# Kernel tuning notes

Measured on AMD Instinct MI355X. Metric: run time of the kernel, lower is better.

Reference implementation:

```python
import jax, jax.numpy as jnp
import numpy as np

NUM_STEPS = 32
SEQ = 64
IN = 512
HID = 256
NUM_CLASSES = 10
BATCH = 2048


def _lstm_layer(xseq, Wih, Whh, bih, bhh):
    # xseq: (T, B, D). PyTorch LSTMCell gate order: i, f, g, o.
    B = xseq.shape[1]
    H = Whh.shape[1]
    h0 = jnp.zeros((B, H), xseq.dtype)
    c0 = jnp.zeros((B, H), xseq.dtype)
    b = bih + bhh

    def step(carry, x):
        h, c = carry
        gates = x @ Wih.T + h @ Whh.T + b  # (B, 4H)
        i, f, g, o = jnp.split(gates, 4, axis=-1)
        c_new = jax.nn.sigmoid(f) * c + jax.nn.sigmoid(i) * jnp.tanh(g)
        h_new = jax.nn.sigmoid(o) * jnp.tanh(c_new)
        return (h_new, c_new), h_new

    (hT, cT), hs = jax.lax.scan(step, (h0, c0), xseq)
    return hs, hT


def _run_stack(xseq, layer_params):
    hT = None
    for (Wih, Whh, bih, bhh) in layer_params:
        xseq, hT = _lstm_layer(xseq, Wih, Whh, bih, bhh)
    return hT


def setup_inputs() -> dict:
    key = jax.random.key(0)
    ks = jax.random.split(key, 32)
    d = {"xs": jax.random.normal(ks[0], (BATCH, SEQ, IN), dtype=jnp.float32)}
    cfg = [IN, HID, HID]
    ki = 1
    for direc in ("f", "r"):
        for l, (di, dh) in enumerate(zip(cfg[:-1], cfg[1:])):
            s = 1.0 / np.sqrt(dh)
            d[f"Wih_{direc}{l}"] = jax.random.uniform(ks[ki], (4 * dh, di), minval=-s, maxval=s); ki += 1
            d[f"Whh_{direc}{l}"] = jax.random.uniform(ks[ki], (4 * dh, dh), minval=-s, maxval=s); ki += 1
            d[f"bih_{direc}{l}"] = jax.random.uniform(ks[ki], (4 * dh,), minval=-s, maxval=s); ki += 1
            d[f"bhh_{direc}{l}"] = jax.random.uniform(ks[ki], (4 * dh,), minval=-s, maxval=s); ki += 1
    s = 1.0 / np.sqrt(2 * HID)
    d["W3"] = jax.random.uniform(ks[ki], (NUM_CLASSES, 2 * HID), minval=-s, maxval=s); ki += 1
    d["b3"] = jax.random.uniform(ks[ki], (NUM_CLASSES,), minval=-s, maxval=s)
    return d


def reference(xs, Wih_f0, Whh_f0, bih_f0, bhh_f0, Wih_f1, Whh_f1, bih_f1, bhh_f1,
              Wih_r0, Whh_r0, bih_r0, bhh_r0, Wih_r1, Whh_r1, bih_r1, bhh_r1, W3, b3):
    # forward direction: timesteps 62-NUM_STEPS .. 61
    xf = jnp.transpose(xs[:, 62 - NUM_STEPS:62, :], (1, 0, 2))  # (T, B, D)
    hF = _run_stack(xf, [(Wih_f0, Whh_f0, bih_f0, bhh_f0),
                         (Wih_f1, Whh_f1, bih_f1, bhh_f1)])
    # reverse direction: last 3 frames in order 63, 62, 61
    xr = jnp.transpose(jnp.flip(xs[:, 61:64, :], axis=1), (1, 0, 2))  # (3, B, D)
    hR = _run_stack(xr, [(Wih_r0, Whh_r0, bih_r0, bhh_r0),
                         (Wih_r1, Whh_r1, bih_r1, bhh_r1)])
    latent = jnp.concatenate([hF, hR], axis=1)  # (B, 512)
    return latent @ W3.T + b3
```

## Files before the change

### kernel.cpp

```cpp
#include <hip/hip_runtime.h>
#include <stdint.h>

typedef unsigned short u16;
typedef unsigned long long u64;
typedef __attribute__((ext_vector_type(8)))  short  bf16x8;
typedef __attribute__((ext_vector_type(8)))  u16    u16x8;
typedef __attribute__((ext_vector_type(4)))  float  f32x4;
typedef __attribute__((ext_vector_type(16))) _Float16 f16x16;

#define MFMA_BF16(a,b,c) __builtin_amdgcn_mfma_f32_16x16x32_bf16((a),(b),(c),0,0,0)

#define BATCH   2048
#define FSTEPS  32
#define RSTEPS  3
#define NVF     35

static constexpr size_t HROW32 = 128;
static constexpr size_t HPAR32 = (size_t)BATCH * HROW32;

static constexpr size_t OFF_CTL  = 0;
static constexpr size_t OFF_H0G  = 32768;
static constexpr size_t OFF_H1G  = OFF_H0G + HPAR32 * 2 * 4;
static constexpr size_t OFF_LAT  = OFF_H1G + HPAR32 * 2 * 4;
static constexpr size_t OFF_XP   = OFF_LAT + (size_t)BATCH * 512 * 4;
static constexpr size_t XP_BYTES = (size_t)NVF * BATCH * 1024 * 2;
static constexpr size_t OFF_W0XF = OFF_XP + XP_BYTES;
static constexpr size_t OFF_W0XR = OFF_W0XF + (size_t)1024 * 512 * 2;
static constexpr size_t OFF_P0F  = OFF_W0XR + (size_t)1024 * 512 * 2;
static constexpr size_t OFF_P0R  = OFF_P0F + (size_t)32768 * 16;
static constexpr size_t OFF_P1F  = OFF_P0R + (size_t)32768 * 16;
static constexpr size_t OFF_P1R  = OFF_P1F + (size_t)65536 * 16;
static constexpr size_t OFF_BS0F = OFF_P1R + (size_t)65536 * 16;
static constexpr size_t OFF_BS0R = OFF_BS0F + 4096;
static constexpr size_t OFF_BS1F = OFF_BS0R + 4096;
static constexpr size_t OFF_BS1R = OFF_BS1F + 4096;
static constexpr size_t WS_NEED  = OFF_BS1R + 4096;

__device__ __forceinline__ u16 f2bf(float f) {
    unsigned u = __float_as_uint(f);
    unsigned r = (u + 0x7fffu + ((u >> 16) & 1u)) >> 16;
    return (u16)r;
}
__device__ __forceinline__ float sigm(float x) { return 1.0f / (1.0f + __expf(-x)); }
__device__ __forceinline__ float tanh_fast(float x) {
    float a = fabsf(x);
    float e = __expf(-2.0f * a);
    float t = (1.0f - e) / (1.0f + e);
    return x < 0.0f ? -t : t;
}

__device__ __forceinline__ bf16x8 ldsA(const char* H, int row, int k) {
    int byte = (row << 9) + (k << 1);
    byte ^= (row & 7) << 4;
    return *(const bf16x8*)(H + byte);
}

__device__ __forceinline__ void reload32(char* Hs, const u64* src, int rg, int tid) {
    u64 v[8];
#pragma unroll
    for (int i = 0; i < 8; ++i) {
        int idx = tid + (i << 8);
        v[i] = __hip_atomic_load(src + ((size_t)rg * 32 + (idx >> 6)) * 64 + (idx & 63),
                                 __ATOMIC_RELAXED, __HIP_MEMORY_SCOPE_AGENT);
    }
#pragma unroll
    for (int i = 0; i < 8; ++i) {
        int idx = tid + (i << 8);
        int row = idx >> 6, cu = idx & 63;
        int byte = (row << 9) + (cu << 3);
        byte ^= (row & 7) << 4;
        *(u64*)(Hs + byte) = v[i];
    }
}

__global__ void __launch_bounds__(256)
lstm_seq(const _Float16* __restrict__ xp,
         const u16* __restrict__ P0f_, const u16* __restrict__ P0r_,
         const u16* __restrict__ P1f_, const u16* __restrict__ P1r_,
         const float* __restrict__ bs1f, const float* __restrict__ bs1r,
         unsigned* __restrict__ h0g, unsigned* __restrict__ h1g,
         float* __restrict__ latent, unsigned* __restrict__ ctl)
{
    __shared__ char T0[16384];
    __shared__ char T1[16384];
    const int tid = threadIdx.x, wq = tid >> 6, lane = tid & 63;
    const int bid = blockIdx.x;
    const int colq = bid >> 6;
    const int rg   = bid & 63;
    const int mem  = colq * 4 + wq;
    const int hc   = mem * 16 + (lane & 15);
    const int klane = lane >> 4, q4 = klane << 2;
    unsigned* flag = ctl + (size_t)rg * 64;
    unsigned bcount = 0;

    for (int dir = 0; dir < 2; ++dir) {
        const int nst = dir ? RSTEPS : FSTEPS;
        const int gbase = dir ? FSTEPS : 0;
        const bf16x8* P0v = (const bf16x8*)(dir ? P0r_ : P0f_) + (size_t)mem * (8 * 4 * 64);
        const bf16x8* P1v = (const bf16x8*)(dir ? P1r_ : P1f_) + (size_t)mem * (16 * 4 * 64);
        const float* bs1 = dir ? bs1r : bs1f;
        float b1reg[4];
#pragma unroll
        for (int g = 0; g < 4; ++g) b1reg[g] = bs1[g * 256 + hc];

        float c0[2][4], c1[2][4];
#pragma unroll
        for (int Mt = 0; Mt < 2; ++Mt)
#pragma unroll
            for (int r = 0; r < 4; ++r) { c0[Mt][r] = 0.f; c1[Mt][r] = 0.f; }

        __syncthreads();
#pragma unroll
        for (int i = 0; i < 4; ++i) {
            ((f32x4*)T0)[i * 256 + tid] = (f32x4){0.f, 0.f, 0.f, 0.f};
            ((f32x4*)T1)[i * 256 + tid] = (f32x4){0.f, 0.f, 0.f, 0.f};
        }
        __syncthreads();

        f16x16 xqm[2];
#pragma unroll
        for (int Mt = 0; Mt < 2; ++Mt)
            xqm[Mt] = *(const f16x16*)(xp +
                ((((size_t)gbase * 128 + rg * 2 + Mt) * 16 + mem) * 64 + lane) * 16);

        for (int t = 0; t <= nst; ++t) {
            f32x4 acc1[4][2];
            if (t >= 1) {
#pragma unroll
                for (int g = 0; g < 4; ++g) { acc1[g][0] = (f32x4){0.f,0.f,0.f,0.f}; acc1[g][1] = (f32x4){0.f,0.f,0.f,0.f}; }
#pragma unroll
                for (int kc = 0; kc < 8; ++kc) {
                    bf16x8 a0 = ldsA(T0, (lane & 15),       kc * 32 + klane * 8);
                    bf16x8 a1 = ldsA(T0, 16 + (lane & 15),  kc * 32 + klane * 8);
#pragma unroll
                    for (int g = 0; g < 4; ++g) {
                        bf16x8 b = P1v[(kc * 4 + g) * 64 + lane];
                        acc1[g][0] = MFMA_BF16(a0, b, acc1[g][0]);
                        acc1[g][1] = MFMA_BF16(a1, b, acc1[g][1]);
                    }
                }
                if (t >= 2) {
#pragma unroll
                    for (int kc = 0; kc < 8; ++kc) {
                        bf16x8 a0 = ldsA(T1, (lane & 15),      kc * 32 + klane * 8);
                        bf16x8 a1 = ldsA(T1, 16 + (lane & 15), kc * 32 + klane * 8);
#pragma unroll
                        for (int g = 0; g < 4; ++g) {
                            bf16x8 b = P1v[((kc + 8) * 4 + g) * 64 + lane];
                            acc1[g][0] = MFMA_BF16(a0, b, acc1[g][0]);
                            acc1[g][1] = MFMA_BF16(a1, b, acc1[g][1]);
                        }
                    }
                }
            }

            f32x4 acc0[4][2];
            if (t < nst) {
#pragma unroll
                for (int g = 0; g < 4; ++g) { acc0[g][0] = (f32x4){0.f,0.f,0.f,0.f}; acc0[g][1] = (f32x4){0.f,0.f,0.f,0.f}; }
                if (t >= 1) {
#pragma unroll
                    for (int kc = 0; kc < 8; ++kc) {
                        bf16x8 a0 = ldsA(T0, (lane & 15),      kc * 32 + klane * 8);
                        bf16x8 a1 = ldsA(T0, 16 + (lane & 15), kc * 32 + klane * 8);
#pragma unroll
                        for (int g = 0; g < 4; ++g) {
                            bf16x8 b = P0v[(kc * 4 + g) * 64 + lane];
                            acc0[g][0] = MFMA_BF16(a0, b, acc0[g][0]);
                            acc0[g][1] = MFMA_BF16(a1, b, acc0[g][1]);
                        }
                    }
                }
            }

            if (t < nst) {
                unsigned* dst = h0g + (size_t)(t & 1) * HPAR32;
                const int cp = mem * 8 + ((lane & 15) >> 1);
#pragma unroll
                for (int Mt = 0; Mt < 2; ++Mt) {
                    float hn[4];
#pragma unroll
                    for (int r = 0; r < 4; ++r) {
                        float gi = acc0[0][Mt][r] + (float)xqm[Mt][0 * 4 + r];
                        float gf = acc0[1][Mt][r] + (float)xqm[Mt][1 * 4 + r];
                        float gg = acc0[2][Mt][r] + (float)xqm[Mt][2 * 4 + r];
                        float go = acc0[3][Mt][r] + (float)xqm[Mt][3 * 4 + r];
                        float cn = sigm(gf) * c0[Mt][r] + sigm(gi) * tanh_fast(gg);
                        c0[Mt][r] = cn;
                        hn[r] = sigm(go) * tanh_fast(cn);
                    }
                    const int rowbase = rg * 32 + Mt * 16 + q4;
#pragma unroll
                    for (int r = 0; r < 4; ++r) {
                        float p = __shfl_xor(hn[r], 1);
                        if (!(lane & 1)) {
                            unsigned w = (unsigned)f2bf(hn[r]) | ((unsigned)f2bf(p) << 16);
                            __hip_atomic_store(dst + (size_t)(rowbase + r) * HROW32 + cp, w,
                                               __ATOMIC_RELAXED, __HIP_MEMORY_SCOPE_AGENT);
                        }
                    }
                }
            }

            if (t >= 1) {
                const int cp = mem * 8 + ((lane & 15) >> 1);
#pragma unroll
                for (int Mt = 0; Mt < 2; ++Mt) {
                    float hn[4];
#pragma unroll
                    for (int r = 0; r < 4; ++r) {
                        float gi = acc1[0][Mt][r] + b1reg[0];
                        float gf = acc1[1][Mt][r] + b1reg[1];
                        float gg = acc1[2][Mt][r] + b1reg[2];
                        float go = acc1[3][Mt][r] + b1reg[3];
                        float cn = sigm(gf) * c1[Mt][r] + sigm(gi) * tanh_fast(gg);
                        c1[Mt][r] = cn;
                        hn[r] = sigm(go) * tanh_fast(cn);
                    }
                    const int rowbase = rg * 32 + Mt * 16 + q4;
                    if (t < nst) {
                        unsigned* dst = h1g + (size_t)((t - 1) & 1) * HPAR32;
#pragma unroll
                        for (int r = 0; r < 4; ++r) {
                            float p = __shfl_xor(hn[r], 1);
                            if (!(lane & 1)) {
                                unsigned w = (unsigned)f2bf(hn[r]) | ((unsigned)f2bf(p) << 16);
                                __hip_atomic_store(dst + (size_t)(rowbase + r) * HROW32 + cp, w,
                                                   __ATOMIC_RELAXED, __HIP_MEMORY_SCOPE_AGENT);
                            }
                        }
                    } else {
#pragma unroll
                        for (int r = 0; r < 4; ++r)
                            latent[(size_t)(rowbase + r) * 512 + dir * 256 + hc] = hn[r];
                    }
                }
            }

            if (t < nst) {
                ++bcount;
                asm volatile("s_waitcnt vmcnt(0)" ::: "memory");
                __syncthreads();
                if (tid == 0)
                    __hip_atomic_fetch_add(flag, 1u, __ATOMIC_RELAXED, __HIP_MEMORY_SCOPE_AGENT);
                if (t + 1 < nst) {
#pragma unroll
                    for (int Mt = 0; Mt < 2; ++Mt)
                        xqm[Mt] = *(const f16x16*)(xp +
                            ((((size_t)(gbase + t + 1) * 128 + rg * 2 + Mt) * 16 + mem) * 64 + lane) * 16);
                }
                if (tid == 0) {
                    while (__hip_atomic_load(flag, __ATOMIC_RELAXED, __HIP_MEMORY_SCOPE_AGENT)
                           < 4u * bcount) {}
                }
                __syncthreads();
                __builtin_amdgcn_sched_barrier(0);
                reload32(T0, (const u64*)(h0g + (size_t)(t & 1) * HPAR32), rg, tid);
                if (t >= 1)
                    reload32(T1, (const u64*)(h1g + (size_t)((t - 1) & 1) * HPAR32), rg, tid);
                __syncthreads();
            }
        }
    }
}

__global__ void __launch_bounds__(256)
xproj_gemm(const float* __restrict__ xs,
           const u16* __restrict__ W0xf, const u16* __restrict__ W0xr,
           const float* __restrict__ bs0f, const float* __restrict__ bs0r,
           _Float16* __restrict__ xp)
{
    __shared__ char As[16384];
    __shared__ char Bs[16384];
    const int tid = threadIdx.x, wv = tid >> 6, lane = tid & 63;
    const int phys = blockIdx.x;
    const int xcd = phys & 7, idx = phys >> 3;
    const int mt = xcd * 70 + (idx >> 3);
    const int nt = idx & 7;
    const int vf = mt >> 4;
    const int dirr = (vf >= 32);
    const int frame = dirr ? (95 - vf) : (30 + vf);
    const int brow = (mt & 15) * 128;
    const u16* Wp = (dirr ? W0xr : W0xf) + (size_t)nt * 128 * 512;
    const float* bs = dirr ? bs0r : bs0f;

    float breg[8];
#pragma unroll
    for (int n = 0; n < 8; ++n) breg[n] = bs[nt * 128 + n * 16 + (lane & 15)];

    f32x4 acc[8][2];
#pragma unroll
    for (int n = 0; n < 8; ++n) { acc[n][0] = (f32x4){0.f,0.f,0.f,0.f}; acc[n][1] = (f32x4){0.f,0.f,0.f,0.f}; }

    const int ar = tid >> 1, akoff = (tid & 1) * 32;
    const float* asrc0 = xs + ((size_t)(brow + ar) * 64 + frame) * 512 + akoff;

    for (int c = 0; c < 8; ++c) {
        {
            const float* s = asrc0 + c * 64;
            u16x8 o[4];
#pragma unroll
            for (int j2 = 0; j2 < 4; ++j2) {
                float4 f0 = *(const float4*)(s + j2 * 8);
                float4 f1 = *(const float4*)(s + j2 * 8 + 4);
                u16x8 o_;
                o_[0] = f2bf(f0.x); o_[1] = f2bf(f0.y); o_[2] = f2bf(f0.z); o_[3] = f2bf(f0.w);
                o_[4] = f2bf(f1.x); o_[5] = f2bf(f1.y); o_[6] = f2bf(f1.z); o_[7] = f2bf(f1.w);
                o[j2] = o_;
            }
#pragma unroll
            for (int j2 = 0; j2 < 4; ++j2) {
                int k = akoff + j2 * 8;
                int byte = (ar << 7) + (k << 1); byte ^= (ar & 7) << 4;
                *(u16x8*)(As + byte) = o[j2];
            }
        }
#pragma unroll
        for (int i = 0; i < 4; ++i) {
            int u = tid + i * 256;
            int ns = u >> 3, c8 = (u & 7) << 3;
            u16x8 v = *(const u16x8*)(Wp + (size_t)ns * 512 + c * 64 + c8);
            int byte = (ns << 7) + (c8 << 1); byte ^= (ns & 7) << 4;
            *(u16x8*)(Bs + byte) = v;
        }
        __syncthreads();
#pragma unroll
        for (int kk = 0; kk < 2; ++kk) {
            int kin = kk * 32 + (lane >> 4) * 8;
            bf16x8 a0, a1;
            int row = wv * 32 + (lane & 15);
            int byte = (row << 7) + (kin << 1); byte ^= (row & 7) << 4;
            a0 = *(const bf16x8*)(As + byte);
            int row1 = row + 16;
            byte = (row1 << 7) + (kin << 1); byte ^= (row1 & 7) << 4;
            a1 = *(const bf16x8*)(As + byte);
#pragma unroll
            for (int n = 0; n < 8; ++n) {
                int ns = n * 16 + (lane & 15);
                int bb = (ns << 7) + (kin << 1); bb ^= (ns & 7) << 4;
                bf16x8 bf_ = *(const bf16x8*)(Bs + bb);
                acc[n][0] = MFMA_BF16(a0, bf_, acc[n][0]);
                acc[n][1] = MFMA_BF16(a1, bf_, acc[n][1]);
            }
        }
        __syncthreads();
    }
#pragma unroll
    for (int n = 0; n < 8; ++n)
#pragma unroll
        for (int mm = 0; mm < 2; ++mm)
#pragma unroll
            for (int r = 0; r < 4; ++r) {
                int vm  = mt * 128 + wv * 32 + mm * 16 + ((lane >> 4) << 2) + r;
                int col = nt * 128 + n * 16 + (lane & 15);
                int vf2 = vm >> 11, brow2 = vm & 2047;
                int rb2 = brow2 >> 4, sub = brow2 & 15;
                int lane2 = ((sub >> 2) << 4) + (col & 15);
                int m2 = (col >> 4) & 15, g2 = col >> 8;
                size_t o = ((((size_t)vf2 * 128 + rb2) * 16 + m2) * 64 + lane2) * 16
                           + (g2 << 2) + (sub & 3);
                xp[o] = (_Float16)(acc[n][mm][r] + breg[n]);
            }
}

__global__ void pack_w(const float* __restrict__ Wa, int da,
                       const float* __restrict__ bi, const float* __restrict__ bh,
                       u16* __restrict__ Wout, float* __restrict__ bout)
{
    int total = 1024 * da;
    int gt = blockIdx.x * blockDim.x + threadIdx.x;
    int stride = gridDim.x * blockDim.x;
    for (int i = gt; i < total; i += stride) Wout[i] = f2bf(Wa[i]);
    if (bout && gt < 1024) bout[gt] = bi[gt] + bh[gt];
}

__global__ void pack_frag(const float* __restrict__ Wa, int da,
                          const float* __restrict__ Wb, int db,
                          int nkc, u16* __restrict__ out,
                          const float* __restrict__ bi, const float* __restrict__ bh,
                          float* __restrict__ bout)
{
    int total = 16 * nkc * 4 * 64;
    int gt = blockIdx.x * blockDim.x + threadIdx.x;
    int stride = gridDim.x * blockDim.x;
    for (int u = gt; u < total; u += stride) {
        int l = u & 63;
        int t1 = u >> 6;
        int g = t1 & 3;
        int t2 = t1 >> 2;
        int kc = t2 % nkc;
        int mem = t2 / nkc;
        int row = g * 256 + mem * 16 + (l & 15);
        int k0 = kc * 32 + ((l >> 4) << 3);
        u16x8 o;
#pragma unroll
        for (int jj = 0; jj < 8; ++jj) {
            int k = k0 + jj;
            float v = (k < da) ? Wa[(size_t)row * da + k] : Wb[(size_t)row * db + (k - da)];
            o[jj] = f2bf(v);
        }
        *(u16x8*)(out + (size_t)u * 8) = o;
    }
    if (bout && gt < 1024) bout[gt] = bi[gt] + bh[gt];
}

__global__ void final_linear(const float* __restrict__ latent, const float* __restrict__ W3,
                             const float* __restrict__ b3, float* __restrict__ out)
{
    int idx = blockIdx.x * blockDim.x + threadIdx.x;
    if (idx >= BATCH * 10) return;
    int bb = idx / 10, c = idx - bb * 10;
    const float* lrow = latent + (size_t)bb * 512;
    const float* wrow = W3 + (size_t)c * 512;
    float s = b3[c];
#pragma unroll 4
    for (int k = 0; k < 512; k += 4) {
        float4 lv = *(const float4*)(lrow + k);
        float4 wv = *(const float4*)(wrow + k);
        s += lv.x * wv.x + lv.y * wv.y + lv.z * wv.z + lv.w * wv.w;
    }
    out[idx] = s;
}

extern "C" void kernel_launch(void* const* d_in, const int* in_sizes, int n_in,
                              void* d_out, int out_size, void* d_ws, size_t ws_size,
                              hipStream_t stream)
{
    (void)in_sizes; (void)n_in; (void)out_size;
    if (ws_size < WS_NEED) return;

    const float* xs     = (const float*)d_in[0];
    const float* Wih_f0 = (const float*)d_in[1];
    const float* Whh_f0 = (const float*)d_in[2];
    const float* bih_f0 = (const float*)d_in[3];
    const float* bhh_f0 = (const float*)d_in[4];
    const float* Wih_f1 = (const float*)d_in[5];
    const float* Whh_f1 = (const float*)d_in[6];
    const float* bih_f1 = (const float*)d_in[7];
    const float* bhh_f1 = (const float*)d_in[8];
    const float* Wih_r0 = (const float*)d_in[9];
    const float* Whh_r0 = (const float*)d_in[10];
    const float* bih_r0 = (const float*)d_in[11];
    const float* bhh_r0 = (const float*)d_in[12];
    const float* Wih_r1 = (const float*)d_in[13];
    const float* Whh_r1 = (const float*)d_in[14];
    const float* bih_r1 = (const float*)d_in[15];
    const float* bhh_r1 = (const float*)d_in[16];
    const float* W3     = (const float*)d_in[17];
    const float* b3     = (const float*)d_in[18];

    char* ws = (char*)d_ws;
    unsigned* ctl = (unsigned*)(ws + OFF_CTL);
    unsigned* h0g = (unsigned*)(ws + OFF_H0G);
    unsigned* h1g = (unsigned*)(ws + OFF_H1G);
    float* latent = (float*)(ws + OFF_LAT);
    _Float16* xp  = (_Float16*)(ws + OFF_XP);
    u16* W0xf = (u16*)(ws + OFF_W0XF);
    u16* W0xr = (u16*)(ws + OFF_W0XR);
    u16* P0f  = (u16*)(ws + OFF_P0F);
    u16* P0r  = (u16*)(ws + OFF_P0R);
    u16* P1f  = (u16*)(ws + OFF_P1F);
    u16* P1r  = (u16*)(ws + OFF_P1R);
    float* bs0f = (float*)(ws + OFF_BS0F);
    float* bs0r = (float*)(ws + OFF_BS0R);
    float* bs1f = (float*)(ws + OFF_BS1F);
    float* bs1r = (float*)(ws + OFF_BS1R);

    hipMemsetAsync(ctl, 0, 32768, stream);

    pack_w<<<256, 256, 0, stream>>>(Wih_f0, 512, bih_f0, bhh_f0, W0xf, bs0f);
    pack_w<<<256, 256, 0, stream>>>(Wih_r0, 512, bih_r0, bhh_r0, W0xr, bs0r);
    pack_frag<<<64, 256, 0, stream>>>(Whh_f0, 256, Whh_f0, 0, 8,  P0f, nullptr, nullptr, nullptr);
    pack_frag<<<64, 256, 0, stream>>>(Whh_r0, 256, Whh_r0, 0, 8,  P0r, nullptr, nullptr, nullptr);
    pack_frag<<<64, 256, 0, stream>>>(Wih_f1, 256, Whh_f1, 256, 16, P1f, bih_f1, bhh_f1, bs1f);
    pack_frag<<<64, 256, 0, stream>>>(Wih_r1, 256, Whh_r1, 256, 16, P1r, bih_r1, bhh_r1, bs1r);

    xproj_gemm<<<4480, 256, 0, stream>>>(xs, W0xf, W0xr, bs0f, bs0r, xp);

    lstm_seq<<<256, 256, 0, stream>>>(xp, P0f, P0r, P1f, P1r, bs1f, bs1r,
                                      h0g, h1g, latent, ctl);

    final_linear<<<80, 256, 0, stream>>>(latent, W3, b3, (float*)d_out);
}
```

Measured before the change: 871.1 us.

## Fuse layer-0 input projection into persistent LSTM kernel, drop xproj GEMM

```diff
diff --git a/kernel.cpp b/kernel.cpp
--- a/kernel.cpp
+++ b/kernel.cpp
@@ -6,14 +6,12 @@
 typedef __attribute__((ext_vector_type(8)))  short  bf16x8;
 typedef __attribute__((ext_vector_type(8)))  u16    u16x8;
 typedef __attribute__((ext_vector_type(4)))  float  f32x4;
-typedef __attribute__((ext_vector_type(16))) _Float16 f16x16;
 
 #define MFMA_BF16(a,b,c) __builtin_amdgcn_mfma_f32_16x16x32_bf16((a),(b),(c),0,0,0)
 
 #define BATCH   2048
 #define FSTEPS  32
 #define RSTEPS  3
-#define NVF     35
 
 static constexpr size_t HROW32 = 128;
 static constexpr size_t HPAR32 = (size_t)BATCH * HROW32;
@@ -22,13 +20,11 @@
 static constexpr size_t OFF_H0G  = 32768;
 static constexpr size_t OFF_H1G  = OFF_H0G + HPAR32 * 2 * 4;
 static constexpr size_t OFF_LAT  = OFF_H1G + HPAR32 * 2 * 4;
-static constexpr size_t OFF_XP   = OFF_LAT + (size_t)BATCH * 512 * 4;
-static constexpr size_t XP_BYTES = (size_t)NVF * BATCH * 1024 * 2;
-static constexpr size_t OFF_W0XF = OFF_XP + XP_BYTES;
-static constexpr size_t OFF_W0XR = OFF_W0XF + (size_t)1024 * 512 * 2;
-static constexpr size_t OFF_P0F  = OFF_W0XR + (size_t)1024 * 512 * 2;
-static constexpr size_t OFF_P0R  = OFF_P0F + (size_t)32768 * 16;
-static constexpr size_t OFF_P1F  = OFF_P0R + (size_t)32768 * 16;
+static constexpr size_t OFF_P0XF = OFF_LAT + (size_t)BATCH * 512 * 4;
+static constexpr size_t OFF_P0XR = OFF_P0XF + (size_t)65536 * 16;
+static constexpr size_t OFF_P0HF = OFF_P0XR + (size_t)65536 * 16;
+static constexpr size_t OFF_P0HR = OFF_P0HF + (size_t)32768 * 16;
+static constexpr size_t OFF_P1F  = OFF_P0HR + (size_t)32768 * 16;
 static constexpr size_t OFF_P1R  = OFF_P1F + (size_t)65536 * 16;
 static constexpr size_t OFF_BS0F = OFF_P1R + (size_t)65536 * 16;
 static constexpr size_t OFF_BS0R = OFF_BS0F + 4096;
@@ -54,6 +50,11 @@
     byte ^= (row & 7) << 4;
     return *(const bf16x8*)(H + byte);
 }
+__device__ __forceinline__ bf16x8 ldsX(const char* X, int row, int k) {
+    int byte = (row << 10) + (k << 1);
+    byte ^= (row & 7) << 4;
+    return *(const bf16x8*)(X + byte);
+}
 
 __device__ __forceinline__ void reload32(char* Hs, const u64* src, int rg, int tid) {
     u64 v[8];
@@ -73,16 +74,45 @@
     }
 }
 
+__device__ __forceinline__ void stageX(char* X, const float* xbase, int tid) {
+#pragma unroll
+    for (int half = 0; half < 2; ++half) {
+        float4 v[8];
+#pragma unroll
+        for (int i = 0; i < 8; ++i) {
+            int u = tid + ((half * 8 + i) << 8);
+            int row = u >> 7, qk = u & 127;
+            v[i] = *(const float4*)(xbase + (size_t)row * 32768 + qk * 4);
+        }
+#pragma unroll
+        for (int i = 0; i < 8; ++i) {
+            int u = tid + ((half * 8 + i) << 8);
+            int row = u >> 7, qk = u & 127;
+            u64 pk = (u64)f2bf(v[i].x) | ((u64)f2bf(v[i].y) << 16)
+                   | ((u64)f2bf(v[i].z) << 32) | ((u64)f2bf(v[i].w) << 48);
+            int byte = (row << 10) + (qk << 3);
+            byte ^= (row & 7) << 4;
+            *(u64*)(X + byte) = pk;
+        }
+    }
+}
+
 __global__ void __launch_bounds__(256)
-lstm_seq(const _Float16* __restrict__ xp,
-         const u16* __restrict__ P0f_, const u16* __restrict__ P0r_,
-         const u16* __restrict__ P1f_, const u16* __restrict__ P1r_,
+lstm_seq(const float* __restrict__ xs,
+         const u16* __restrict__ P0xf_, const u16* __restrict__ P0xr_,
+         const u16* __restrict__ P0hf_, const u16* __restrict__ P0hr_,
+         const u16* __restrict__ P1f_,  const u16* __restrict__ P1r_,
+         const float* __restrict__ bs0f, const float* __restrict__ bs0r,
          const float* __restrict__ bs1f, const float* __restrict__ bs1r,
          unsigned* __restrict__ h0g, unsigned* __restrict__ h1g,
          float* __restrict__ latent, unsigned* __restrict__ ctl)
 {
-    __shared__ char T0[16384];
-    __shared__ char T1[16384];
+    extern __shared__ char lds[];
+    char* T0 = lds;
+    char* T1 = lds + 16384;
+    char* X0 = lds + 32768;
+    char* X1 = lds + 65536;
+
     const int tid = threadIdx.x, wq = tid >> 6, lane = tid & 63;
     const int bid = blockIdx.x;
     const int colq = bid >> 6;
@@ -95,13 +125,14 @@
 
     for (int dir = 0; dir < 2; ++dir) {
         const int nst = dir ? RSTEPS : FSTEPS;
-        const int gbase = dir ? FSTEPS : 0;
-        const bf16x8* P0v = (const bf16x8*)(dir ? P0r_ : P0f_) + (size_t)mem * (8 * 4 * 64);
-        const bf16x8* P1v = (const bf16x8*)(dir ? P1r_ : P1f_) + (size_t)mem * (16 * 4 * 64);
+        const bf16x8* P0xv = (const bf16x8*)(dir ? P0xr_ : P0xf_) + (size_t)mem * (16 * 4 * 64);
+        const bf16x8* P0hv = (const bf16x8*)(dir ? P0hr_ : P0hf_) + (size_t)mem * (8 * 4 * 64);
+        const bf16x8* P1v  = (const bf16x8*)(dir ? P1r_  : P1f_)  + (size_t)mem * (16 * 4 * 64);
+        const float* bs0 = dir ? bs0r : bs0f;
         const float* bs1 = dir ? bs1r : bs1f;
-        float b1reg[4];
-#pragma unroll
-        for (int g = 0; g < 4; ++g) b1reg[g] = bs1[g * 256 + hc];
+        float b0reg[4], b1reg[4];
+#pragma unroll
+        for (int g = 0; g < 4; ++g) { b0reg[g] = bs0[g * 256 + hc]; b1reg[g] = bs1[g * 256 + hc]; }
 
         float c0[2][4], c1[2][4];
 #pragma unroll
@@ -116,14 +147,12 @@
             ((f32x4*)T1)[i * 256 + tid] = (f32x4){0.f, 0.f, 0.f, 0.f};
         }
         __syncthreads();
-
-        f16x16 xqm[2];
-#pragma unroll
-        for (int Mt = 0; Mt < 2; ++Mt)
-            xqm[Mt] = *(const f16x16*)(xp +
-                ((((size_t)gbase * 128 + rg * 2 + Mt) * 16 + mem) * 64 + lane) * 16);
+        stageX(X0, xs + ((size_t)(rg * 32) * 64 + (dir ? 63 : 30)) * 512, tid);
+        __syncthreads();
 
         for (int t = 0; t <= nst; ++t) {
+            const char* Xc = (t & 1) ? X1 : X0;
+
             f32x4 acc1[4][2];
             if (t >= 1) {
 #pragma unroll
@@ -158,6 +187,17 @@
             if (t < nst) {
 #pragma unroll
                 for (int g = 0; g < 4; ++g) { acc0[g][0] = (f32x4){0.f,0.f,0.f,0.f}; acc0[g][1] = (f32x4){0.f,0.f,0.f,0.f}; }
+#pragma unroll
+                for (int kc = 0; kc < 16; ++kc) {
+                    bf16x8 a0 = ldsX(Xc, (lane & 15),      kc * 32 + klane * 8);
+                    bf16x8 a1 = ldsX(Xc, 16 + (lane & 15), kc * 32 + klane * 8);
+#pragma unroll
+                    for (int g = 0; g < 4; ++g) {
+                        bf16x8 b = P0xv[(kc * 4 + g) * 64 + lane];
+                        acc0[g][0] = MFMA_BF16(a0, b, acc0[g][0]);
+                        acc0[g][1] = MFMA_BF16(a1, b, acc0[g][1]);
+                    }
+                }
                 if (t >= 1) {
 #pragma unroll
                     for (int kc = 0; kc < 8; ++kc) {
@@ -165,7 +205,7 @@
                         bf16x8 a1 = ldsA(T0, 16 + (lane & 15), kc * 32 + klane * 8);
 #pragma unroll
                         for (int g = 0; g < 4; ++g) {
-                            bf16x8 b = P0v[(kc * 4 + g) * 64 + lane];
+                            bf16x8 b = P0hv[(kc * 4 + g) * 64 + lane];
                             acc0[g][0] = MFMA_BF16(a0, b, acc0[g][0]);
                             acc0[g][1] = MFMA_BF16(a1, b, acc0[g][1]);
                         }
@@ -181,10 +221,10 @@
                     float hn[4];
 #pragma unroll
                     for (int r = 0; r < 4; ++r) {
-                        float gi = acc0[0][Mt][r] + (float)xqm[Mt][0 * 4 + r];
-                        float gf = acc0[1][Mt][r] + (float)xqm[Mt][1 * 4 + r];
-                        float gg = acc0[2][Mt][r] + (float)xqm[Mt][2 * 4 + r];
-                        float go = acc0[3][Mt][r] + (float)xqm[Mt][3 * 4 + r];
+                        float gi = acc0[0][Mt][r] + b0reg[0];
+                        float gf = acc0[1][Mt][r] + b0reg[1];
+                        float gg = acc0[2][Mt][r] + b0reg[2];
+                        float go = acc0[3][Mt][r] + b0reg[3];
                         float cn = sigm(gf) * c0[Mt][r] + sigm(gi) * tanh_fast(gg);
                         c0[Mt][r] = cn;
                         hn[r] = sigm(go) * tanh_fast(cn);
@@ -194,8 +234,8 @@
                     for (int r = 0; r < 4; ++r) {
                         float p = __shfl_xor(hn[r], 1);
                         if (!(lane & 1)) {
-                            unsigned w = (unsigned)f2bf(hn[r]) | ((unsigned)f2bf(p) << 16);
-                            __hip_atomic_store(dst + (size_t)(rowbase + r) * HROW32 + cp, w,
+                            unsigned wv_ = (unsigned)f2bf(hn[r]) | ((unsigned)f2bf(p) << 16);
+                            __hip_atomic_store(dst + (size_t)(rowbase + r) * HROW32 + cp, wv_,
                                                __ATOMIC_RELAXED, __HIP_MEMORY_SCOPE_AGENT);
                         }
                     }
@@ -224,8 +264,8 @@
                         for (int r = 0; r < 4; ++r) {
                             float p = __shfl_xor(hn[r], 1);
                             if (!(lane & 1)) {
-                                unsigned w = (unsigned)f2bf(hn[r]) | ((unsigned)f2bf(p) << 16);
-                                __hip_atomic_store(dst + (size_t)(rowbase + r) * HROW32 + cp, w,
+                                unsigned wv_ = (unsigned)f2bf(hn[r]) | ((unsigned)f2bf(p) << 16);
+                                __hip_atomic_store(dst + (size_t)(rowbase + r) * HROW32 + cp, wv_,
                                                    __ATOMIC_RELAXED, __HIP_MEMORY_SCOPE_AGENT);
                             }
                         }
@@ -244,10 +284,9 @@
                 if (tid == 0)
                     __hip_atomic_fetch_add(flag, 1u, __ATOMIC_RELAXED, __HIP_MEMORY_SCOPE_AGENT);
                 if (t + 1 < nst) {
-#pragma unroll
-                    for (int Mt = 0; Mt < 2; ++Mt)
-                        xqm[Mt] = *(const f16x16*)(xp +
-                            ((((size_t)(gbase + t + 1) * 128 + rg * 2 + Mt) * 16 + mem) * 64 + lane) * 16);
+                    const int frame = dir ? (62 - t) : (31 + t);
+                    stageX((t & 1) ? X0 : X1,
+                           xs + ((size_t)(rg * 32) * 64 + frame) * 512, tid);
                 }
                 if (tid == 0) {
                     while (__hip_atomic_load(flag, __ATOMIC_RELAXED, __HIP_MEMORY_SCOPE_AGENT)
@@ -262,116 +301,6 @@
             }
         }
     }
-}
-
-__global__ void __launch_bounds__(256)
-xproj_gemm(const float* __restrict__ xs,
-           const u16* __restrict__ W0xf, const u16* __restrict__ W0xr,
-           const float* __restrict__ bs0f, const float* __restrict__ bs0r,
-           _Float16* __restrict__ xp)
-{
-    __shared__ char As[16384];
-    __shared__ char Bs[16384];
-    const int tid = threadIdx.x, wv = tid >> 6, lane = tid & 63;
-    const int phys = blockIdx.x;
-    const int xcd = phys & 7, idx = phys >> 3;
-    const int mt = xcd * 70 + (idx >> 3);
-    const int nt = idx & 7;
-    const int vf = mt >> 4;
-    const int dirr = (vf >= 32);
-    const int frame = dirr ? (95 - vf) : (30 + vf);
-    const int brow = (mt & 15) * 128;
-    const u16* Wp = (dirr ? W0xr : W0xf) + (size_t)nt * 128 * 512;
-    const float* bs = dirr ? bs0r : bs0f;
-
-    float breg[8];
-#pragma unroll
-    for (int n = 0; n < 8; ++n) breg[n] = bs[nt * 128 + n * 16 + (lane & 15)];
-
-    f32x4 acc[8][2];
-#pragma unroll
-    for (int n = 0; n < 8; ++n) { acc[n][0] = (f32x4){0.f,0.f,0.f,0.f}; acc[n][1] = (f32x4){0.f,0.f,0.f,0.f}; }
-
-    const int ar = tid >> 1, akoff = (tid & 1) * 32;
-    const float* asrc0 = xs + ((size_t)(brow + ar) * 64 + frame) * 512 + akoff;
-
-    for (int c = 0; c < 8; ++c) {
-        {
-            const float* s = asrc0 + c * 64;
-            u16x8 o[4];
-#pragma unroll
-            for (int j2 = 0; j2 < 4; ++j2) {
-                float4 f0 = *(const float4*)(s + j2 * 8);
-                float4 f1 = *(const float4*)(s + j2 * 8 + 4);
-                u16x8 o_;
-                o_[0] = f2bf(f0.x); o_[1] = f2bf(f0.y); o_[2] = f2bf(f0.z); o_[3] = f2bf(f0.w);
-                o_[4] = f2bf(f1.x); o_[5] = f2bf(f1.y); o_[6] = f2bf(f1.z); o_[7] = f2bf(f1.w);
-                o[j2] = o_;
-            }
-#pragma unroll
-            for (int j2 = 0; j2 < 4; ++j2) {
-                int k = akoff + j2 * 8;
-                int byte = (ar << 7) + (k << 1); byte ^= (ar & 7) << 4;
-                *(u16x8*)(As + byte) = o[j2];
-            }
-        }
-#pragma unroll
-        for (int i = 0; i < 4; ++i) {
-            int u = tid + i * 256;
-            int ns = u >> 3, c8 = (u & 7) << 3;
-            u16x8 v = *(const u16x8*)(Wp + (size_t)ns * 512 + c * 64 + c8);
-            int byte = (ns << 7) + (c8 << 1); byte ^= (ns & 7) << 4;
-            *(u16x8*)(Bs + byte) = v;
-        }
-        __syncthreads();
-#pragma unroll
-        for (int kk = 0; kk < 2; ++kk) {
-            int kin = kk * 32 + (lane >> 4) * 8;
-            bf16x8 a0, a1;
-            int row = wv * 32 + (lane & 15);
-            int byte = (row << 7) + (kin << 1); byte ^= (row & 7) << 4;
-            a0 = *(const bf16x8*)(As + byte);
-            int row1 = row + 16;
-            byte = (row1 << 7) + (kin << 1); byte ^= (row1 & 7) << 4;
-            a1 = *(const bf16x8*)(As + byte);
-#pragma unroll
-            for (int n = 0; n < 8; ++n) {
-                int ns = n * 16 + (lane & 15);
-                int bb = (ns << 7) + (kin << 1); bb ^= (ns & 7) << 4;
-                bf16x8 bf_ = *(const bf16x8*)(Bs + bb);
-                acc[n][0] = MFMA_BF16(a0, bf_, acc[n][0]);
-                acc[n][1] = MFMA_BF16(a1, bf_, acc[n][1]);
-            }
-        }
-        __syncthreads();
-    }
-#pragma unroll
-    for (int n = 0; n < 8; ++n)
-#pragma unroll
-        for (int mm = 0; mm < 2; ++mm)
-#pragma unroll
-            for (int r = 0; r < 4; ++r) {
-                int vm  = mt * 128 + wv * 32 + mm * 16 + ((lane >> 4) << 2) + r;
-                int col = nt * 128 + n * 16 + (lane & 15);
-                int vf2 = vm >> 11, brow2 = vm & 2047;
-                int rb2 = brow2 >> 4, sub = brow2 & 15;
-                int lane2 = ((sub >> 2) << 4) + (col & 15);
-                int m2 = (col >> 4) & 15, g2 = col >> 8;
-                size_t o = ((((size_t)vf2 * 128 + rb2) * 16 + m2) * 64 + lane2) * 16
-                           + (g2 << 2) + (sub & 3);
-                xp[o] = (_Float16)(acc[n][mm][r] + breg[n]);
-            }
-}
-
-__global__ void pack_w(const float* __restrict__ Wa, int da,
-                       const float* __restrict__ bi, const float* __restrict__ bh,
-                       u16* __restrict__ Wout, float* __restrict__ bout)
-{
-    int total = 1024 * da;
-    int gt = blockIdx.x * blockDim.x + threadIdx.x;
-    int stride = gridDim.x * blockDim.x;
-    for (int i = gt; i < total; i += stride) Wout[i] = f2bf(Wa[i]);
-    if (bout && gt < 1024) bout[gt] = bi[gt] + bh[gt];
 }
 
 __global__ void pack_frag(const float* __restrict__ Wa, int da,
@@ -454,11 +383,10 @@
     unsigned* h0g = (unsigned*)(ws + OFF_H0G);
     unsigned* h1g = (unsigned*)(ws + OFF_H1G);
     float* latent = (float*)(ws + OFF_LAT);
-    _Float16* xp  = (_Float16*)(ws + OFF_XP);
-    u16* W0xf = (u16*)(ws + OFF_W0XF);
-    u16* W0xr = (u16*)(ws + OFF_W0XR);
-    u16* P0f  = (u16*)(ws + OFF_P0F);
-    u16* P0r  = (u16*)(ws + OFF_P0R);
+    u16* P0xf = (u16*)(ws + OFF_P0XF);
+    u16* P0xr = (u16*)(ws + OFF_P0XR);
+    u16* P0hf = (u16*)(ws + OFF_P0HF);
+    u16* P0hr = (u16*)(ws + OFF_P0HR);
     u16* P1f  = (u16*)(ws + OFF_P1F);
     u16* P1r  = (u16*)(ws + OFF_P1R);
     float* bs0f = (float*)(ws + OFF_BS0F);
@@ -468,17 +396,18 @@
 
     hipMemsetAsync(ctl, 0, 32768, stream);
 
-    pack_w<<<256, 256, 0, stream>>>(Wih_f0, 512, bih_f0, bhh_f0, W0xf, bs0f);
-    pack_w<<<256, 256, 0, stream>>>(Wih_r0, 512, bih_r0, bhh_r0, W0xr, bs0r);
-    pack_frag<<<64, 256, 0, stream>>>(Whh_f0, 256, Whh_f0, 0, 8,  P0f, nullptr, nullptr, nullptr);
-    pack_frag<<<64, 256, 0, stream>>>(Whh_r0, 256, Whh_r0, 0, 8,  P0r, nullptr, nullptr, nullptr);
+    pack_frag<<<64, 256, 0, stream>>>(Wih_f0, 512, Wih_f0, 0, 16, P0xf, bih_f0, bhh_f0, bs0f);
+    pack_frag<<<64, 256, 0, stream>>>(Wih_r0, 512, Wih_r0, 0, 16, P0xr, bih_r0, bhh_r0, bs0r);
+    pack_frag<<<64, 256, 0, stream>>>(Whh_f0, 256, Whh_f0, 0, 8,  P0hf, nullptr, nullptr, nullptr);
+    pack_frag<<<64, 256, 0, stream>>>(Whh_r0, 256, Whh_r0, 0, 8,  P0hr, nullptr, nullptr, nullptr);
     pack_frag<<<64, 256, 0, stream>>>(Wih_f1, 256, Whh_f1, 256, 16, P1f, bih_f1, bhh_f1, bs1f);
     pack_frag<<<64, 256, 0, stream>>>(Wih_r1, 256, Whh_r1, 256, 16, P1r, bih_r1, bhh_r1, bs1r);
 
-    xproj_gemm<<<4480, 256, 0, stream>>>(xs, W0xf, W0xr, bs0f, bs0r, xp);
-
-    lstm_seq<<<256, 256, 0, stream>>>(xp, P0f, P0r, P1f, P1r, bs1f, bs1r,
-                                      h0g, h1g, latent, ctl);
+    hipFuncSetAttribute((const void*)lstm_seq,
+                        hipFuncAttributeMaxDynamicSharedMemorySize, 98304);
+    lstm_seq<<<256, 256, 98304, stream>>>(xs, P0xf, P0xr, P0hf, P0hr, P1f, P1r,
+                                          bs0f, bs0r, bs1f, bs1r,
+                                          h0g, h1g, latent, ctl);
 
     final_linear<<<80, 256, 0, stream>>>(latent, W3, b3, (float*)d_out);
 }
```

Measured after the change: 1.687 ms. 93.7% more time.
